# Kernel optimization log

Measured on AMD Instinct MI355X. Metric: run time of the kernel, lower is better.

Reference implementation:

```python
import jax, jax.numpy as jnp
import numpy as np

VTHR = 1.0


def setup_inputs() -> dict:
    key = jax.random.key(0)
    k1, k2, k3 = jax.random.split(key, 3)
    B, T, IN, OUT = 256, 8, 4096, 4096
    x = jax.random.normal(k1, (B * T, IN), dtype=jnp.float32)
    weight_scaled = jax.random.normal(k2, (OUT, IN), dtype=jnp.float32) * 0.02
    bias_scaled = jax.random.normal(k3, (OUT,), dtype=jnp.float32) * 0.02
    return {"x": x, "weight_scaled": weight_scaled, "bias_scaled": bias_scaled, "timesteps": T}


def _spike_linear(x, weight_scaled, bias_scaled, timesteps):
    # F.linear: [B*T, IN] @ [OUT, IN]^T + [OUT]
    out = jnp.dot(x, weight_scaled.T) + bias_scaled  # [B*T, OUT]
    OUT = out.shape[-1]
    out_s = out.reshape(-1, timesteps, OUT)  # [B, T, OUT]
    out_t = jnp.transpose(out_s, (1, 0, 2))  # [T, B, OUT] for scan

    def step(memb, o_t):
        memb = memb + VTHR * o_t
        spike = (memb > VTHR).astype(out.dtype)
        memb = memb * (1.0 - spike)  # reset_mode == 'zero'
        return memb, spike

    memb0 = jnp.zeros(out_t.shape[1:], dtype=out.dtype)
    _, spikes = jax.lax.scan(step, memb0, out_t)  # [T, B, OUT]
    # torch.cat(spikes, 0): t-major concat -> [T*B, OUT]
    return spikes.reshape(-1, OUT)


def reference(x, weight_scaled, bias_scaled, timesteps):
    return _spike_linear(x, weight_scaled, bias_scaled, timesteps)
```

## Files before the change

kernel.cpp:

```cpp
#include <hip/hip_runtime.h>


constexpr int TSTEPS = 8;
constexpr int BK     = 16;
constexpr int TILE_M = 64;
constexpr int TILE_N = 128;
constexpr int KC     = 384;

__global__ __launch_bounds__(256, 4)
void spike_linear_f32seq(const float* __restrict__ x,
                         const float* __restrict__ w,
                         const float* __restrict__ bias,
                         float* __restrict__ out,
                         int B, int IN, int OUT)
{
    __shared__ float xs[BK][TILE_M + 4];
    __shared__ float ws[BK][TILE_N + 4];

    const int tid = threadIdx.x;
    const int tx  = tid & 31;
    const int ty  = tid >> 5;

    const int m0 = blockIdx.y * TILE_M;
    const int n0 = blockIdx.x * TILE_N;

    float acc_tot[TSTEPS][4];
    float acc_blk[TSTEPS][4];
    #pragma unroll
    for (int t = 0; t < TSTEPS; ++t)
        #pragma unroll
        for (int c = 0; c < 4; ++c) { acc_tot[t][c] = 0.f; acc_blk[t][c] = 0.f; }

    const int sr = tid >> 2;
    const int sk = (tid & 3) * 4;

    const float* xrow  = x + (size_t)(m0 + sr) * IN + sk;
    const float* wrow0 = w + (size_t)(n0 + sr) * IN + sk;
    const float* wrow1 = w + (size_t)(n0 + 64 + sr) * IN + sk;

    for (int kk = 0; kk < IN; kk += BK) {
        if (kk > 0 && (kk % KC) == 0) {
            #pragma unroll
            for (int t = 0; t < TSTEPS; ++t)
                #pragma unroll
                for (int c = 0; c < 4; ++c) {
                    acc_tot[t][c] += acc_blk[t][c];
                    acc_blk[t][c] = 0.f;
                }
        }

        const float4 xv  = *(const float4*)(xrow  + kk);
        const float4 wv0 = *(const float4*)(wrow0 + kk);
        const float4 wv1 = *(const float4*)(wrow1 + kk);
        __syncthreads();
        xs[sk+0][sr] = xv.x;  xs[sk+1][sr] = xv.y;
        xs[sk+2][sr] = xv.z;  xs[sk+3][sr] = xv.w;
        ws[sk+0][sr] = wv0.x; ws[sk+1][sr] = wv0.y;
        ws[sk+2][sr] = wv0.z; ws[sk+3][sr] = wv0.w;
        ws[sk+0][sr+64] = wv1.x; ws[sk+1][sr+64] = wv1.y;
        ws[sk+2][sr+64] = wv1.z; ws[sk+3][sr+64] = wv1.w;
        __syncthreads();

        #pragma unroll
        for (int k = 0; k < BK; ++k) {
            float xr[TSTEPS];
            *(float4*)&xr[0] = *(const float4*)&xs[k][ty*8];
            *(float4*)&xr[4] = *(const float4*)&xs[k][ty*8 + 4];
            float wr[4];
            *(float4*)&wr[0] = *(const float4*)&ws[k][tx*4];
            #pragma unroll
            for (int t = 0; t < TSTEPS; ++t)
                #pragma unroll
                for (int c = 0; c < 4; ++c)
                    acc_blk[t][c] = fmaf(xr[t], wr[c], acc_blk[t][c]);
        }
    }
    #pragma unroll
    for (int t = 0; t < TSTEPS; ++t)
        #pragma unroll
        for (int c = 0; c < 4; ++c)
            acc_tot[t][c] += acc_blk[t][c];

    const int bg = blockIdx.y * 8 + ty;
    const int o0 = n0 + tx * 4;
    const float4 bv = *(const float4*)(bias + o0);
    const float bb[4] = {bv.x, bv.y, bv.z, bv.w};
    float memb[4] = {0.f, 0.f, 0.f, 0.f};
    #pragma unroll
    for (int t = 0; t < TSTEPS; ++t) {
        float4 sp;
        float* spp = (float*)&sp;
        #pragma unroll
        for (int c = 0; c < 4; ++c) {
            float pre = acc_tot[t][c] + bb[c];
            memb[c] += pre;
            float s = (memb[c] > 1.0f) ? 1.0f : 0.0f;
            memb[c] *= (1.0f - s);
            spp[c] = s;
        }
        *(float4*)(out + ((size_t)t * B + bg) * OUT + o0) = sp;
    }
}

extern "C" void kernel_launch(void* const* d_in, const int* in_sizes, int n_in,
                              void* d_out, int out_size, void* d_ws, size_t ws_size,
                              hipStream_t stream)
{
    const float* x    = (const float*)d_in[0];
    const float* w    = (const float*)d_in[1];
    const float* bias = (const float*)d_in[2];
    float* out = (float*)d_out;

    const int OUT = in_sizes[2];
    const int IN  = in_sizes[1] / OUT;
    const int BT  = in_sizes[0] / IN;
    const int B   = BT / TSTEPS;

    dim3 grid(OUT / TILE_N, BT / TILE_M);
    spike_linear_f32seq<<<grid, 256, 0, stream>>>(x, w, bias, out, B, IN, OUT);
}
```

Before: 851.3 us.

## Split K into panels across blocks and fold partial sums in a scan kernel

Adds a split-K path. One GEMM launch spreads the K dimension over a third grid axis of KC-sized panels and writes each panel's partial sums to workspace; the last panel writes to the output buffer. A second kernel then adds the panels in the same order as the sequential block fold, adds bias, and runs the spiking scan. The aim is more blocks and shorter per-block K loops, at the cost of a very large workspace (about ten full-size output copies) written and read back through global memory. When the workspace is too small, the original fused kernel is used instead.

```diff
diff --git a/kernel.cpp b/kernel.cpp
--- a/kernel.cpp
+++ b/kernel.cpp
@@ -6,6 +6,131 @@
 constexpr int TILE_M = 64;
 constexpr int TILE_N = 128;
 constexpr int KC     = 384;
+constexpr int FOLD_S = KC / BK;
+
+__global__ __launch_bounds__(256, 4)
+void spike_panel_gemm(const float* __restrict__ x,
+                      const float* __restrict__ w,
+                      const float* __restrict__ bias,
+                      float* __restrict__ panels,
+                      float* __restrict__ out,
+                      int B, int IN, int OUT, int npanels)
+{
+    __shared__ float xs[BK][TILE_M + 4];
+    __shared__ float wsh[BK][TILE_N + 4];
+
+    const int tid = threadIdx.x;
+    const int tx  = tid & 31;
+    const int ty  = tid >> 5;
+
+    const int m0 = blockIdx.y * TILE_M;
+    const int n0 = blockIdx.x * TILE_N;
+    const int p  = blockIdx.z;
+    const int ks = p * KC;
+    const int ke = (ks + KC < IN) ? (ks + KC) : IN;
+
+    float acc[TSTEPS][4];
+    #pragma unroll
+    for (int t = 0; t < TSTEPS; ++t)
+        #pragma unroll
+        for (int c = 0; c < 4; ++c) acc[t][c] = 0.f;
+
+    const int sr = tid >> 2;
+    const int sk = (tid & 3) * 4;
+
+    const float* xrow  = x + (size_t)(m0 + sr) * IN + sk;
+    const float* wrow0 = w + (size_t)(n0 + sr) * IN + sk;
+    const float* wrow1 = w + (size_t)(n0 + 64 + sr) * IN + sk;
+
+    for (int kk = ks; kk < ke; kk += BK) {
+        const float4 xv  = *(const float4*)(xrow  + kk);
+        const float4 wv0 = *(const float4*)(wrow0 + kk);
+        const float4 wv1 = *(const float4*)(wrow1 + kk);
+        __syncthreads();
+        xs[sk+0][sr] = xv.x;  xs[sk+1][sr] = xv.y;
+        xs[sk+2][sr] = xv.z;  xs[sk+3][sr] = xv.w;
+        wsh[sk+0][sr]    = wv0.x; wsh[sk+1][sr]    = wv0.y;
+        wsh[sk+2][sr]    = wv0.z; wsh[sk+3][sr]    = wv0.w;
+        wsh[sk+0][sr+64] = wv1.x; wsh[sk+1][sr+64] = wv1.y;
+        wsh[sk+2][sr+64] = wv1.z; wsh[sk+3][sr+64] = wv1.w;
+        __syncthreads();
+
+        #pragma unroll
+        for (int k = 0; k < BK; ++k) {
+            float xr[TSTEPS];
+            *(float4*)&xr[0] = *(const float4*)&xs[k][ty*8];
+            *(float4*)&xr[4] = *(const float4*)&xs[k][ty*8 + 4];
+            float wr[4];
+            *(float4*)&wr[0] = *(const float4*)&wsh[k][tx*4];
+            #pragma unroll
+            for (int t = 0; t < TSTEPS; ++t)
+                #pragma unroll
+                for (int c = 0; c < 4; ++c)
+                    acc[t][c] = fmaf(xr[t], wr[c], acc[t][c]);
+        }
+    }
+
+    const int bg = blockIdx.y * 8 + ty;
+    const int o0 = n0 + tx * 4;
+    if (p < npanels - 1) {
+        float* pb = panels + (size_t)p * B * TSTEPS * OUT;
+        #pragma unroll
+        for (int t = 0; t < TSTEPS; ++t) {
+            const int m = bg * TSTEPS + t;
+            *(float4*)(pb + (size_t)m * OUT + o0) = *(float4*)&acc[t][0];
+        }
+    } else {
+        #pragma unroll
+        for (int t = 0; t < TSTEPS; ++t)
+            *(float4*)(out + ((size_t)t * B + bg) * OUT + o0) = *(float4*)&acc[t][0];
+    }
+}
+
+__global__ __launch_bounds__(256)
+void spike_fold_scan(const float* __restrict__ panels,
+                     const float* __restrict__ bias,
+                     float* __restrict__ out,
+                     int B, int OUT, int npanels)
+{
+    const int col = blockIdx.x * 1024 + threadIdx.x * 4;
+    const int b   = blockIdx.y;
+    const size_t psz = (size_t)B * TSTEPS * OUT;
+
+    float4 v[TSTEPS];
+    #pragma unroll
+    for (int t = 0; t < TSTEPS; ++t)
+        v[t] = *(const float4*)(panels + (size_t)(b*TSTEPS + t) * OUT + col);
+    for (int p = 1; p < npanels - 1; ++p) {
+        const float* pb = panels + (size_t)p * psz;
+        #pragma unroll
+        for (int t = 0; t < TSTEPS; ++t) {
+            const float4 u = *(const float4*)(pb + (size_t)(b*TSTEPS + t) * OUT + col);
+            v[t].x += u.x; v[t].y += u.y; v[t].z += u.z; v[t].w += u.w;
+        }
+    }
+    #pragma unroll
+    for (int t = 0; t < TSTEPS; ++t) {
+        const float4 u = *(const float4*)(out + ((size_t)t * B + b) * OUT + col);
+        v[t].x += u.x; v[t].y += u.y; v[t].z += u.z; v[t].w += u.w;
+    }
+
+    const float4 bb = *(const float4*)(bias + col);
+    float memb[4] = {0.f, 0.f, 0.f, 0.f};
+    #pragma unroll
+    for (int t = 0; t < TSTEPS; ++t) {
+        float pre[4] = {v[t].x + bb.x, v[t].y + bb.y, v[t].z + bb.z, v[t].w + bb.w};
+        float4 sp;
+        float* spp = (float*)&sp;
+        #pragma unroll
+        for (int c = 0; c < 4; ++c) {
+            memb[c] += pre[c];
+            float s = (memb[c] > 1.0f) ? 1.0f : 0.0f;
+            memb[c] *= (1.0f - s);
+            spp[c] = s;
+        }
+        *(float4*)(out + ((size_t)t * B + b) * OUT + col) = sp;
+    }
+}
 
 __global__ __launch_bounds__(256, 4)
 void spike_linear_f32seq(const float* __restrict__ x,
@@ -48,15 +173,14 @@
                     acc_blk[t][c] = 0.f;
                 }
         }
-
         const float4 xv  = *(const float4*)(xrow  + kk);
         const float4 wv0 = *(const float4*)(wrow0 + kk);
         const float4 wv1 = *(const float4*)(wrow1 + kk);
         __syncthreads();
         xs[sk+0][sr] = xv.x;  xs[sk+1][sr] = xv.y;
         xs[sk+2][sr] = xv.z;  xs[sk+3][sr] = xv.w;
-        ws[sk+0][sr] = wv0.x; ws[sk+1][sr] = wv0.y;
-        ws[sk+2][sr] = wv0.z; ws[sk+3][sr] = wv0.w;
+        ws[sk+0][sr]    = wv0.x; ws[sk+1][sr]    = wv0.y;
+        ws[sk+2][sr]    = wv0.z; ws[sk+3][sr]    = wv0.w;
         ws[sk+0][sr+64] = wv1.x; ws[sk+1][sr+64] = wv1.y;
         ws[sk+2][sr+64] = wv1.z; ws[sk+3][sr+64] = wv1.w;
         __syncthreads();
@@ -116,6 +240,18 @@
     const int BT  = in_sizes[0] / IN;
     const int B   = BT / TSTEPS;
 
-    dim3 grid(OUT / TILE_N, BT / TILE_M);
-    spike_linear_f32seq<<<grid, 256, 0, stream>>>(x, w, bias, out, B, IN, OUT);
-}
+    const int npanels = (IN + KC - 1) / KC;
+    const size_t need = (size_t)(npanels - 1) * BT * OUT * sizeof(float);
+
+    if (ws_size >= need && (OUT % 1024) == 0) {
+        float* panels = (float*)d_ws;
+        dim3 g1(OUT / TILE_N, BT / TILE_M, npanels);
+        spike_panel_gemm<<<g1, 256, 0, stream>>>(x, w, bias, panels, out,
+                                                 B, IN, OUT, npanels);
+        dim3 g2(OUT / 1024, B);
+        spike_fold_scan<<<g2, 256, 0, stream>>>(panels, bias, out, B, OUT, npanels);
+    } else {
+        dim3 grid(OUT / TILE_N, BT / TILE_M);
+        spike_linear_f32seq<<<grid, 256, 0, stream>>>(x, w, bias, out, B, IN, OUT);
+    }
+}
```

New measurement: 852.1 us. About the same (+0.1%).
